# Performance work log

Measured on AMD Instinct MI355X. Metric: run time of the kernel, lower is better.

## Reference

```python
import jax, jax.numpy as jnp
import numpy as np


def setup_inputs() -> dict:
    key = jax.random.key(0)
    k1, k2, k3 = jax.random.split(key, 3)
    N, C, W = 32, 64, 4096
    F, WW = 128, 64
    x = jax.random.normal(k1, (N, C, W), dtype=jnp.float32)
    w = jax.random.normal(k2, (F, C, WW), dtype=jnp.float32)
    b = jax.random.normal(k3, (F,), dtype=jnp.float32)
    return {"x": x, "w": w, "b": b}


def reference(x, w, b):
    # FFT-based 1D cross-correlation (the original loops over N, F, C; here batched).
    # x: [N, C, W], w: [F, C, WW], b: [F]
    N, C, W = x.shape
    F, _, WW = w.shape
    pad = 0  # module's padding kwarg
    fftsize = 1 << int(np.ceil(np.log2(W + 2 * pad + WW - 1)))  # next_power2
    out_W = W + 2 * pad - WW + 1
    # rfft of zero-padded signals and filters
    xfft = jnp.fft.rfft(x, n=fftsize, axis=-1)          # [N, C, K]
    wfft = jnp.fft.rfft(w, n=fftsize, axis=-1)          # [F, C, K]
    # cross-correlation: multiply by conj of filter spectrum, sum over channels
    offt = jnp.einsum('nck,fck->nfk', xfft, jnp.conj(wfft))  # [N, F, K]
    out = jnp.fft.irfft(offt, n=fftsize, axis=-1)[..., :out_W]  # real part, first out_W samples
    return out + b[None, :, None]
```

## Files before the change

### kernel.cpp

```cpp
#include <hip/hip_runtime.h>


#define C_TOT   64
#define F_TOT   128
#define KW      64
#define OUT_W   4033
#define W_IN    4096
#define N_BATCH 32
#define T_BLK   256
#define XROWS   320
#define XSTR    72
#define TRS     260
#define BK_SH   8192

typedef __attribute__((ext_vector_type(8))) short  short8;
typedef __attribute__((ext_vector_type(4))) float  floatx4;

__device__ inline unsigned short f32_to_bf16(float f) {
  unsigned int u = __float_as_uint(f);
  u += 0x7FFF + ((u >> 16) & 1);
  return (unsigned short)(u >> 16);
}

__device__ inline void async16(const unsigned short* g, unsigned short* l) {
  __builtin_amdgcn_global_load_lds(
      (const __attribute__((address_space(1))) unsigned int*)g,
      (__attribute__((address_space(3))) unsigned int*)l, 16, 0, 0);
}

__global__ __launch_bounds__(256) void conv1d_prep(
    const float* __restrict__ w, unsigned short* __restrict__ wsw) {
  int i4 = blockIdx.x * 256 + threadIdx.x;
  if (i4 < F_TOT * C_TOT * KW / 4) {
    int c4 = (i4 & 15) * 4;
    int f  = (i4 >> 4) & 127;
    int k  = i4 >> 11;
    const float* src = w + ((size_t)f * C_TOT + c4) * KW + k;
    ushort4 o;
    o.x = f32_to_bf16(src[0 * KW]);
    o.y = f32_to_bf16(src[1 * KW]);
    o.z = f32_to_bf16(src[2 * KW]);
    o.w = f32_to_bf16(src[3 * KW]);
    int chunk = (c4 >> 3) ^ (f & 7);
    *(ushort4*)&wsw[((size_t)(k * F_TOT + f) * 8 + chunk) * 8 + (c4 & 7)] = o;
  }
}

__global__ __launch_bounds__(256, 2) void conv1d_mfma(
    const float* __restrict__ x, const unsigned short* __restrict__ wsw,
    const float* __restrict__ b, float* __restrict__ out) {
  __shared__ union SM {
    unsigned short xt[XROWS * XSTR];
    float tr[32 * TRS];
  } sm;
  __shared__ unsigned short bls[2][BK_SH];

  const int tid  = threadIdx.x;
  const int lane = tid & 63;
  const int wv   = tid >> 6;
  const int q    = lane >> 4;
  const int col  = lane & 15;
  const int n    = blockIdx.y;
  const int t0   = blockIdx.x * T_BLK;
  const int fh2  = wv & 1;
  const int th   = wv >> 1;

  const float* xrowb = x + (size_t)n * C_TOT * W_IN;

  floatx4 acc[8][4];
#pragma unroll
  for (int ms = 0; ms < 8; ++ms)
#pragma unroll
    for (int ft = 0; ft < 4; ++ft) acc[ms][ft] = (floatx4)0.0f;

#define STAGE_B(k_, p_)                                                        \
  {                                                                            \
    const unsigned short* wb = wsw + (size_t)(k_) * BK_SH;                     \
    _Pragma("unroll")                                                          \
    for (int s = 0; s < 4; ++s) {                                              \
      int off = ((wv * 4 + s) * 64 + lane) * 8;                                \
      async16(wb + off, &bls[p_][off]);                                        \
    }                                                                          \
  }

  STAGE_B(0, 0)
#pragma unroll 4
  for (int it = 0; it < 20; ++it) {
    int j  = it * 256 + tid;
    int c  = j / 80;
    int tq = j - c * 80;
    int gt = t0 + tq * 4;
    const float* src = xrowb + (size_t)c * W_IN + gt;
    float4 v = {0.f, 0.f, 0.f, 0.f};
    if (gt + 3 < W_IN) v = *(const float4*)src;
    else {
      if (gt < W_IN)     v.x = src[0];
      if (gt + 1 < W_IN) v.y = src[1];
      if (gt + 2 < W_IN) v.z = src[2];
    }
    int rb = tq * 4;
    sm.xt[(rb + 0) * XSTR + c] = f32_to_bf16(v.x);
    sm.xt[(rb + 1) * XSTR + c] = f32_to_bf16(v.y);
    sm.xt[(rb + 2) * XSTR + c] = f32_to_bf16(v.z);
    sm.xt[(rb + 3) * XSTR + c] = f32_to_bf16(v.w);
  }
  __syncthreads();

#pragma unroll 2
  for (int k = 0; k < KW; ++k) {
    const int p = k & 1;
    if (k + 1 < KW) STAGE_B(k + 1, p ^ 1)

    const unsigned short* xk = &sm.xt[(th * 128 + col + k) * XSTR + q * 8];
    const unsigned short* bp = &bls[p][(fh2 * 64 + col) * 64];

#pragma unroll
    for (int cstep = 0; cstep < 2; ++cstep) {
      short8 Bf[4];
#pragma unroll
      for (int ft = 0; ft < 4; ++ft)
        Bf[ft] = *(const short8*)&bp[ft * 1024 + (((cstep << 2) + q) ^ (col & 7)) * 8];
#pragma unroll
      for (int ms = 0; ms < 8; ++ms) {
        const short8 Af = *(const short8*)&xk[ms * 16 * XSTR + cstep * 32];
#pragma unroll
        for (int ft = 0; ft < 4; ++ft)
          acc[ms][ft] =
              __builtin_amdgcn_mfma_f32_16x16x32_bf16(Af, Bf[ft], acc[ms][ft], 0, 0, 0);
      }
    }
    __syncthreads();
  }

  const int fs_w  = fh2 * 16 + col;
  const int fs_r  = tid >> 3;
  const int seg   = tid & 7;
  const int f_r   = (fs_r >> 4) * 64 + (fs_r & 15);
  const size_t ob = ((size_t)n * F_TOT) * OUT_W;

#pragma unroll
  for (int j = 0; j < 4; ++j) {
#pragma unroll
    for (int ms = 0; ms < 8; ++ms) {
      float4 vv;
      vv.x = acc[ms][j][0];
      vv.y = acc[ms][j][1];
      vv.z = acc[ms][j][2];
      vv.w = acc[ms][j][3];
      int tl = 128 * th + 16 * ms + 4 * q;
      *(float4*)&sm.tr[fs_w * TRS + tl] = vv;
    }
    __syncthreads();
    const int f = f_r + 16 * j;
    const float bias = b[f];
    const size_t obf = ob + (size_t)f * OUT_W;
#pragma unroll
    for (int j2 = 0; j2 < 8; ++j2) {
      int tl = seg * 4 + 32 * j2;
      float4 vv = *(const float4*)&sm.tr[fs_r * TRS + tl];
      vv.x += bias; vv.y += bias; vv.z += bias; vv.w += bias;
      int t = t0 + tl;
      if (t + 3 < OUT_W) {
        *(float4*)&out[obf + t] = vv;
      } else {
        float e[4] = {vv.x, vv.y, vv.z, vv.w};
#pragma unroll
        for (int u = 0; u < 4; ++u)
          if (t + u < OUT_W) out[obf + t + u] = e[u];
      }
    }
    __syncthreads();
  }
}

extern "C" void kernel_launch(void* const* d_in, const int* in_sizes, int n_in,
                              void* d_out, int out_size, void* d_ws, size_t ws_size,
                              hipStream_t stream) {
  const float* x = (const float*)d_in[0];
  const float* w = (const float*)d_in[1];
  const float* b = (const float*)d_in[2];
  float* out = (float*)d_out;

  unsigned short* wsw = (unsigned short*)d_ws;

  conv1d_prep<<<(F_TOT * C_TOT * KW / 4 + 255) / 256, 256, 0, stream>>>(w, wsw);

  dim3 grid((OUT_W + T_BLK - 1) / T_BLK, N_BATCH);
  conv1d_mfma<<<grid, 256, 0, stream>>>(x, wsw, b, out);
}
```

Before: 197.5 us.

## Split channels into halves and pair taps to reuse A fragments across MFMAs

The loop order changes from 64 taps × 64 channels to 64 groups, each covering 32 channels and a pair of taps (k and k+16). Nine A fragments are loaded once and shared across both taps by shifting the row index by 16. The x tile now holds only 32 channels at a time with a narrower stride, and the second half is restaged midway, which shrinks LDS and cuts A-fragment reads per MFMA. The weight prep layout is rewritten to match. In exchange it adds an extra staging barrier and a strided, non-vectorized global load pattern for x.

```diff
diff --git a/kernel.cpp b/kernel.cpp
--- a/kernel.cpp
+++ b/kernel.cpp
@@ -1,17 +1,18 @@
 #include <hip/hip_runtime.h>
 
 
-#define C_TOT   64
-#define F_TOT   128
-#define KW      64
-#define OUT_W   4033
-#define W_IN    4096
-#define N_BATCH 32
-#define T_BLK   256
-#define XROWS   320
-#define XSTR    72
-#define TRS     260
-#define BK_SH   8192
+#define C_TOT    64
+#define F_TOT    128
+#define KW       64
+#define OUT_W    4033
+#define W_IN     4096
+#define N_BATCH  32
+#define T_BLK    256
+#define XROWS    320
+#define XSTR     40
+#define WROW     40
+#define TRS      260
+#define CHUNK_SH 10240
 
 typedef __attribute__((ext_vector_type(8))) short  short8;
 typedef __attribute__((ext_vector_type(4))) float  floatx4;
@@ -30,19 +31,21 @@
 
 __global__ __launch_bounds__(256) void conv1d_prep(
     const float* __restrict__ w, unsigned short* __restrict__ wsw) {
-  int i4 = blockIdx.x * 256 + threadIdx.x;
-  if (i4 < F_TOT * C_TOT * KW / 4) {
-    int c4 = (i4 & 15) * 4;
-    int f  = (i4 >> 4) & 127;
-    int k  = i4 >> 11;
-    const float* src = w + ((size_t)f * C_TOT + c4) * KW + k;
+  int j = blockIdx.x * 256 + threadIdx.x;
+  if (j < 64 * 2 * 128 * 8) {
+    int c4  = (j & 7) * 4;
+    int f   = (j >> 3) & 127;
+    int tap = (j >> 10) & 1;
+    int gi  = j >> 11;
+    int k   = (gi & 15) + 32 * ((gi >> 4) & 1) + 16 * tap;
+    int cg0 = (gi >> 5) * 32 + c4;
+    const float* src = w + ((size_t)f * C_TOT + cg0) * KW + k;
     ushort4 o;
     o.x = f32_to_bf16(src[0 * KW]);
     o.y = f32_to_bf16(src[1 * KW]);
     o.z = f32_to_bf16(src[2 * KW]);
     o.w = f32_to_bf16(src[3 * KW]);
-    int chunk = (c4 >> 3) ^ (f & 7);
-    *(ushort4*)&wsw[((size_t)(k * F_TOT + f) * 8 + chunk) * 8 + (c4 & 7)] = o;
+    *(ushort4*)&wsw[((size_t)(gi * 2 + tap) * 128 + f) * WROW + c4] = o;
   }
 }
 
@@ -53,13 +56,13 @@
     unsigned short xt[XROWS * XSTR];
     float tr[32 * TRS];
   } sm;
-  __shared__ unsigned short bls[2][BK_SH];
+  __shared__ unsigned short bls[2][CHUNK_SH];
 
   const int tid  = threadIdx.x;
   const int lane = tid & 63;
-  const int wv   = tid >> 6;
   const int q    = lane >> 4;
   const int col  = lane & 15;
+  const int wv   = tid >> 6;
   const int n    = blockIdx.y;
   const int t0   = blockIdx.x * T_BLK;
   const int fh2  = wv & 1;
@@ -73,63 +76,71 @@
 #pragma unroll
     for (int ft = 0; ft < 4; ++ft) acc[ms][ft] = (floatx4)0.0f;
 
-#define STAGE_B(k_, p_)                                                        \
+#define STAGE_W(gi_, p_)                                                       \
   {                                                                            \
-    const unsigned short* wb = wsw + (size_t)(k_) * BK_SH;                     \
+    const unsigned short* wb = wsw + (size_t)(gi_) * CHUNK_SH;                 \
     _Pragma("unroll")                                                          \
-    for (int s = 0; s < 4; ++s) {                                              \
-      int off = ((wv * 4 + s) * 64 + lane) * 8;                                \
+    for (int s = 0; s < 5; ++s) {                                              \
+      int off = (s * 256 + tid) * 8;                                           \
       async16(wb + off, &bls[p_][off]);                                        \
     }                                                                          \
   }
 
-  STAGE_B(0, 0)
-#pragma unroll 4
-  for (int it = 0; it < 20; ++it) {
-    int j  = it * 256 + tid;
-    int c  = j / 80;
-    int tq = j - c * 80;
-    int gt = t0 + tq * 4;
-    const float* src = xrowb + (size_t)c * W_IN + gt;
-    float4 v = {0.f, 0.f, 0.f, 0.f};
-    if (gt + 3 < W_IN) v = *(const float4*)src;
-    else {
-      if (gt < W_IN)     v.x = src[0];
-      if (gt + 1 < W_IN) v.y = src[1];
-      if (gt + 2 < W_IN) v.z = src[2];
-    }
-    int rb = tq * 4;
-    sm.xt[(rb + 0) * XSTR + c] = f32_to_bf16(v.x);
-    sm.xt[(rb + 1) * XSTR + c] = f32_to_bf16(v.y);
-    sm.xt[(rb + 2) * XSTR + c] = f32_to_bf16(v.z);
-    sm.xt[(rb + 3) * XSTR + c] = f32_to_bf16(v.w);
-  }
+#define STAGE_X(hc_)                                                           \
+  {                                                                            \
+    _Pragma("unroll")                                                          \
+    for (int r = 0; r < 10; ++r) {                                             \
+      int ti = (r % 5) * 64 + (tid & 63);                                      \
+      int cl = ((r / 5) * 4 + (tid >> 6)) * 4;                                 \
+      int gt = t0 + ti;                                                        \
+      const float* src = xrowb + (size_t)((hc_) * 32 + cl) * W_IN + gt;        \
+      float4 v = {0.f, 0.f, 0.f, 0.f};                                         \
+      if (gt < W_IN) {                                                         \
+        v.x = src[0];                                                          \
+        v.y = src[W_IN];                                                       \
+        v.z = src[2 * W_IN];                                                   \
+        v.w = src[3 * W_IN];                                                   \
+      }                                                                        \
+      ushort4 o;                                                               \
+      o.x = f32_to_bf16(v.x); o.y = f32_to_bf16(v.y);                          \
+      o.z = f32_to_bf16(v.z); o.w = f32_to_bf16(v.w);                          \
+      *(ushort4*)&sm.xt[ti * XSTR + cl] = o;                                   \
+    }                                                                          \
+  }
+
+  STAGE_W(0, 0)
+  STAGE_X(0)
   __syncthreads();
 
-#pragma unroll 2
-  for (int k = 0; k < KW; ++k) {
-    const int p = k & 1;
-    if (k + 1 < KW) STAGE_B(k + 1, p ^ 1)
-
-    const unsigned short* xk = &sm.xt[(th * 128 + col + k) * XSTR + q * 8];
-    const unsigned short* bp = &bls[p][(fh2 * 64 + col) * 64];
-
-#pragma unroll
-    for (int cstep = 0; cstep < 2; ++cstep) {
-      short8 Bf[4];
-#pragma unroll
-      for (int ft = 0; ft < 4; ++ft)
-        Bf[ft] = *(const short8*)&bp[ft * 1024 + (((cstep << 2) + q) ^ (col & 7)) * 8];
-#pragma unroll
-      for (int ms = 0; ms < 8; ++ms) {
-        const short8 Af = *(const short8*)&xk[ms * 16 * XSTR + cstep * 32];
-#pragma unroll
-        for (int ft = 0; ft < 4; ++ft)
-          acc[ms][ft] =
-              __builtin_amdgcn_mfma_f32_16x16x32_bf16(Af, Bf[ft], acc[ms][ft], 0, 0, 0);
+  for (int gi = 0; gi < 64; ++gi) {
+    const int p = gi & 1;
+    if (gi + 1 < 64) STAGE_W(gi + 1, p ^ 1)
+
+    const int k1 = (gi & 15) + 32 * ((gi >> 4) & 1);
+    const unsigned short* ap = &sm.xt[(128 * th + col + k1) * XSTR + q * 8];
+    const unsigned short* bp = &bls[p][(fh2 * 64 + col) * WROW + q * 8];
+
+    short8 A[9];
+#pragma unroll
+    for (int jj = 0; jj < 9; ++jj)
+      A[jj] = *(const short8*)&ap[jj * 16 * XSTR];
+
+#pragma unroll
+    for (int tap = 0; tap < 2; ++tap) {
+#pragma unroll
+      for (int ft = 0; ft < 4; ++ft) {
+        const short8 B = *(const short8*)&bp[(tap * 128 + ft * 16) * WROW];
+#pragma unroll
+        for (int ms = 0; ms < 8; ++ms)
+          acc[ms][ft] = __builtin_amdgcn_mfma_f32_16x16x32_bf16(
+              A[ms + tap], B, acc[ms][ft], 0, 0, 0);
       }
     }
     __syncthreads();
+    if (gi == 31) {
+      STAGE_X(1)
+      __syncthreads();
+    }
   }
 
   const int fs_w  = fh2 * 16 + col;
@@ -183,7 +194,7 @@
 
   unsigned short* wsw = (unsigned short*)d_ws;
 
-  conv1d_prep<<<(F_TOT * C_TOT * KW / 4 + 255) / 256, 256, 0, stream>>>(w, wsw);
+  conv1d_prep<<<512, 256, 0, stream>>>(w, wsw);
 
   dim3 grid((OUT_W + T_BLK - 1) / T_BLK, N_BATCH);
   conv1d_mfma<<<grid, 256, 0, stream>>>(x, wsw, b, out);
```

Measured after the change: 194.7 us. Within noise of the previous version (-1.4%).
